# Performance work log

Measured on AMD Instinct MI355X. Metric: run time of the kernel, lower is better.

Reference implementation:

```python
import jax, jax.numpy as jnp
import numpy as np

OUT_H, OUT_W = 7, 7
SPATIAL_SCALE = 0.125
SAMPLING_RATIO = 2


def setup_inputs() -> dict:
    key = jax.random.key(0)
    k1, k2, k3, k4 = jax.random.split(key, 4)
    inputs = jax.random.normal(k1, (2, 100, 100, 256), dtype=jnp.float32)
    # boxes in image coords (stride-8 feature over ~800px image): x0,y0,x1,y1
    xy0 = jax.random.uniform(k2, (1024, 2), minval=0.0, maxval=600.0)
    wh = jax.random.uniform(k3, (1024, 2), minval=8.0, maxval=200.0)
    boxes = jnp.concatenate([xy0, xy0 + wh], axis=1).astype(jnp.float32)
    box_inds = jax.random.randint(k4, (1024,), 0, 2, dtype=jnp.int32)
    return {"inputs": inputs, "boxes": boxes, "box_inds": box_inds}


def _roi_align(inputs, boxes, box_inds):
    """aligned=True ROIAlign: crop_and_resize at oversampled grid + avg pool.

    Sample coordinate (per aligned=True transform + tf.crop_and_resize):
      x_j = x0*scale + spacing_w*(j+0.5) - 0.5, spacing_w = w_box*scale/crop_w
    Out-of-range samples get extrapolation_value=0 (TF semantics).
    """
    N, H, W, C = inputs.shape
    B = boxes.shape[0]
    ch, cw = OUT_H * SAMPLING_RATIO, OUT_W * SAMPLING_RATIO

    sb = boxes * SPATIAL_SCALE
    x0, y0, x1, y1 = sb[:, 0], sb[:, 1], sb[:, 2], sb[:, 3]
    sw = (x1 - x0) / cw  # [B]
    sh = (y1 - y0) / ch
    xs = x0[:, None] + sw[:, None] * (jnp.arange(cw, dtype=sb.dtype) + 0.5) - 0.5  # [B,cw]
    ys = y0[:, None] + sh[:, None] * (jnp.arange(ch, dtype=sb.dtype) + 0.5) - 0.5  # [B,ch]

    yl = jnp.floor(ys)
    xl = jnp.floor(xs)
    ty = ys - yl  # [B,ch]
    tx = xs - xl  # [B,cw]
    yli = jnp.clip(yl, 0, H - 1).astype(jnp.int32)
    yhi = jnp.clip(yl + 1, 0, H - 1).astype(jnp.int32)
    xli = jnp.clip(xl, 0, W - 1).astype(jnp.int32)
    xhi = jnp.clip(xl + 1, 0, W - 1).astype(jnp.int32)

    b = box_inds[:, None, None]

    def g(yy, xx):  # gather -> [B,ch,cw,C]
        return inputs[b, yy[:, :, None], xx[:, None, :], :]

    txe = tx[:, None, :, None]
    top = g(yli, xli) * (1.0 - txe) + g(yli, xhi) * txe
    bot = g(yhi, xli) * (1.0 - txe) + g(yhi, xhi) * txe
    tye = ty[:, :, None, None]
    out = top * (1.0 - tye) + bot * tye  # [B,ch,cw,C]

    valid = ((ys >= 0) & (ys <= H - 1))[:, :, None] & ((xs >= 0) & (xs <= W - 1))[:, None, :]
    out = jnp.where(valid[..., None], out, 0.0)

    # avg_pool2d kernel=stride=SAMPLING_RATIO (SAME==VALID since exact multiple)
    out = out.reshape(B, OUT_H, SAMPLING_RATIO, OUT_W, SAMPLING_RATIO, C).mean(axis=(2, 4))
    return out  # [B, OUT_H, OUT_W, C]


def reference(inputs, boxes, box_inds):
    return _roi_align(inputs, boxes, box_inds)
```

## Files before the change

kernel.cpp:

```cpp
#include <hip/hip_runtime.h>


constexpr int   H_IN  = 100;
constexpr int   W_IN  = 100;
constexpr int   C_IN  = 256;
constexpr int   OUT_H = 7;
constexpr int   OUT_W = 7;
constexpr int   SR    = 2;
constexpr int   NPIX  = OUT_H * OUT_W;
constexpr float SCALE = 0.125f;

typedef float f32x4 __attribute__((ext_vector_type(4)));

template<int NR, int NC>
__device__ __forceinline__ f32x4 gather(const float* __restrict__ base,
                                        const int* ro, const int* co,
                                        const float* wr, const float* wc,
                                        int c4)
{
    f32x4 v[NR * NC];
#pragma unroll
    for (int i = 0; i < NR; ++i)
#pragma unroll
        for (int j = 0; j < NC; ++j)
            v[i * NC + j] = *(const f32x4*)(base + (size_t)((ro[i] + co[j]) * C_IN + c4));

    f32x4 acc = {0.f, 0.f, 0.f, 0.f};
#pragma unroll
    for (int i = 0; i < NR; ++i)
#pragma unroll
        for (int j = 0; j < NC; ++j)
            acc += v[i * NC + j] * (wr[i] * wc[j]);
    return acc;
}

__device__ __forceinline__ int merge_dim(float s0, float s1, int LIM,
                                         int* idx, float* w)
{
    const float f0 = floorf(s0);
    const float f1 = floorf(s1);
    const float t0 = s0 - f0;
    const float t1 = s1 - f1;
    const float va = (s0 >= 0.0f && s0 <= (float)(LIM - 1)) ? 1.0f : 0.0f;
    const float vb = (s1 >= 0.0f && s1 <= (float)(LIM - 1)) ? 1.0f : 0.0f;
    const int i0 = (int)f0;
    const int i1 = (int)f1;

    int n;
    if (i1 == i0) {
        n = 2;
        idx[0] = i0;     w[0] = va * (1.0f - t0) + vb * (1.0f - t1);
        idx[1] = i0 + 1; w[1] = va * t0 + vb * t1;
    } else if (i1 == i0 + 1) {
        n = 3;
        idx[0] = i0;     w[0] = va * (1.0f - t0);
        idx[1] = i0 + 1; w[1] = va * t0 + vb * (1.0f - t1);
        idx[2] = i0 + 2; w[2] = vb * t1;
    } else {
        n = 4;
        idx[0] = i0;     w[0] = va * (1.0f - t0);
        idx[1] = i0 + 1; w[1] = va * t0;
        idx[2] = i1;     w[2] = vb * (1.0f - t1);
        idx[3] = i1 + 1; w[3] = vb * t1;
    }
#pragma unroll
    for (int k = 0; k < 4; ++k)
        idx[k] = min(max(idx[k], 0), LIM - 1);
    return n;
}

__global__ __launch_bounds__(256) void roi_align_kernel(
    const float* __restrict__ inputs,
    const float* __restrict__ boxes,
    const int*   __restrict__ box_inds,
    float*       __restrict__ out)
{
    const int tid  = threadIdx.x;
    const int lane = tid & 63;
    const int sub  = tid >> 6;

    const int nchunk = gridDim.x >> 3;
    const int lbid   = (blockIdx.x & 7) * nchunk + (blockIdx.x >> 3);
    const int p      = lbid * 4 + sub;

    const int b   = p / NPIX;
    const int rem = p - b * NPIX;
    const int oy  = rem / OUT_W;
    const int ox  = rem - oy * OUT_W;

    const float x0 = boxes[b * 4 + 0] * SCALE;
    const float y0 = boxes[b * 4 + 1] * SCALE;
    const float x1 = boxes[b * 4 + 2] * SCALE;
    const float y1 = boxes[b * 4 + 3] * SCALE;
    const float sw = (x1 - x0) * (1.0f / (OUT_W * SR));
    const float sh = (y1 - y0) * (1.0f / (OUT_H * SR));
    const int   n  = box_inds[b];

    const float* base = inputs + (size_t)n * (H_IN * W_IN * C_IN);
    const int c4 = lane * 4;

    const float ys0 = y0 + sh * ((float)(oy * SR) + 0.5f) - 0.5f;
    const float ys1 = ys0 + sh;
    int   ridx[4]; float wr[4];
    const int nr = merge_dim(ys0, ys1, H_IN, ridx, wr);
#pragma unroll
    for (int k = 0; k < 4; ++k) ridx[k] *= W_IN;

    const float xs0 = x0 + sw * ((float)(ox * SR) + 0.5f) - 0.5f;
    const float xs1 = xs0 + sw;
    int   cidx[4]; float wc[4];
    const int nc = merge_dim(xs0, xs1, W_IN, cidx, wc);

    const int sel = __builtin_amdgcn_readfirstlane((nr - 2) * 3 + (nc - 2));

    f32x4 acc;
    switch (sel) {
        case 0: acc = gather<2, 2>(base, ridx, cidx, wr, wc, c4); break;
        case 1: acc = gather<2, 3>(base, ridx, cidx, wr, wc, c4); break;
        case 2: acc = gather<2, 4>(base, ridx, cidx, wr, wc, c4); break;
        case 3: acc = gather<3, 2>(base, ridx, cidx, wr, wc, c4); break;
        case 4: acc = gather<3, 3>(base, ridx, cidx, wr, wc, c4); break;
        case 5: acc = gather<3, 4>(base, ridx, cidx, wr, wc, c4); break;
        case 6: acc = gather<4, 2>(base, ridx, cidx, wr, wc, c4); break;
        case 7: acc = gather<4, 3>(base, ridx, cidx, wr, wc, c4); break;
        default: acc = gather<4, 4>(base, ridx, cidx, wr, wc, c4); break;
    }

    acc *= 0.25f;

    float* op = out + (size_t)p * C_IN + c4;
    __builtin_nontemporal_store(acc, (f32x4*)op);
}

extern "C" void kernel_launch(void* const* d_in, const int* in_sizes, int n_in,
                              void* d_out, int out_size, void* d_ws, size_t ws_size,
                              hipStream_t stream) {
    const float* inputs   = (const float*)d_in[0];
    const float* boxes    = (const float*)d_in[1];
    const int*   box_inds = (const int*)d_in[2];
    float*       out      = (float*)d_out;

    const int npix_total = 1024 * NPIX;
    const int blocks     = npix_total / 4;
    roi_align_kernel<<<blocks, 256, 0, stream>>>(inputs, boxes, box_inds, out);
}
```

Measured before the change: 34.95 us.

## Sort boxes by image and vertical band to improve gather cache locality

Adds a single-block pre-pass that buckets the 1024 boxes by batch index and one of four vertical bands of the box centre. It uses wave ballots and a serial prefix sum to write a permutation into workspace. The main kernel then processes boxes in permuted order and scatters results back to their original output slots. The intent is for concurrently running blocks to touch nearby feature-map rows, raising L2/MALL hit rates. The cost is an extra kernel launch with a serialized scan, plus one dependent perm load per thread.

```diff
diff --git a/kernel.cpp b/kernel.cpp
--- a/kernel.cpp
+++ b/kernel.cpp
@@ -8,9 +8,53 @@
 constexpr int   OUT_W = 7;
 constexpr int   SR    = 2;
 constexpr int   NPIX  = OUT_H * OUT_W;
+constexpr int   NBOX  = 1024;
 constexpr float SCALE = 0.125f;
 
 typedef float f32x4 __attribute__((ext_vector_type(4)));
+
+__global__ __launch_bounds__(1024) void sort_boxes_kernel(
+    const float* __restrict__ boxes,
+    const int*   __restrict__ box_inds,
+    int*         __restrict__ perm)
+{
+    const int tid  = threadIdx.x;
+    const int wave = tid >> 6;
+    const int lane = tid & 63;
+
+    const float y0 = boxes[tid * 4 + 1] * SCALE;
+    const float y1 = boxes[tid * 4 + 3] * SCALE;
+    const float cy = 0.5f * (y0 + y1);
+    int band = (int)(cy * (1.0f / 25.0f));
+    band = min(max(band, 0), 3);
+    const int bin = box_inds[tid] * 4 + band;
+
+    __shared__ int whist[16][8];
+    __shared__ int wbase[16][8];
+
+    int wrank = 0;
+    const unsigned long long ltmask = (lane == 63) ? ~0ull >> 1
+                                                   : (1ull << lane) - 1;
+#pragma unroll
+    for (int k = 0; k < 8; ++k) {
+        const unsigned long long bal = __ballot(bin == k);
+        if (bin == k) wrank = __popcll(bal & ltmask);
+        if (lane == 0) whist[wave][k] = __popcll(bal);
+    }
+    __syncthreads();
+
+    if (tid == 0) {
+        int acc = 0;
+        for (int k = 0; k < 8; ++k)
+            for (int w = 0; w < 16; ++w) {
+                wbase[w][k] = acc;
+                acc += whist[w][k];
+            }
+    }
+    __syncthreads();
+
+    perm[wbase[wave][bin] + wrank] = tid;
+}
 
 template<int NR, int NC>
 __device__ __forceinline__ f32x4 gather(const float* __restrict__ base,
@@ -73,6 +117,7 @@
     const float* __restrict__ inputs,
     const float* __restrict__ boxes,
     const int*   __restrict__ box_inds,
+    const int*   __restrict__ perm,
     float*       __restrict__ out)
 {
     const int tid  = threadIdx.x;
@@ -83,8 +128,9 @@
     const int lbid   = (blockIdx.x & 7) * nchunk + (blockIdx.x >> 3);
     const int p      = lbid * 4 + sub;
 
-    const int b   = p / NPIX;
-    const int rem = p - b * NPIX;
+    const int bs  = p / NPIX;
+    const int b   = perm[bs];
+    const int rem = p - bs * NPIX;
     const int oy  = rem / OUT_W;
     const int ox  = rem - oy * OUT_W;
 
@@ -128,7 +174,7 @@
 
     acc *= 0.25f;
 
-    float* op = out + (size_t)p * C_IN + c4;
+    float* op = out + (size_t)b * (NPIX * C_IN) + (size_t)rem * C_IN + c4;
     __builtin_nontemporal_store(acc, (f32x4*)op);
 }
 
@@ -139,8 +185,11 @@
     const float* boxes    = (const float*)d_in[1];
     const int*   box_inds = (const int*)d_in[2];
     float*       out      = (float*)d_out;
+    int*         perm     = (int*)d_ws;
 
-    const int npix_total = 1024 * NPIX;
+    sort_boxes_kernel<<<1, NBOX, 0, stream>>>(boxes, box_inds, perm);
+
+    const int npix_total = NBOX * NPIX;
     const int blocks     = npix_total / 4;
-    roi_align_kernel<<<blocks, 256, 0, stream>>>(inputs, boxes, box_inds, out);
+    roi_align_kernel<<<blocks, 256, 0, stream>>>(inputs, boxes, box_inds, perm, out);
 }
```

New measurement: 31.78 us. 1.1x faster.
